# Performance work log

Measured on AMD Instinct MI355X. Metric: run time of the kernel, lower is better.

The kernel has to match this reference:

```python
import jax, jax.numpy as jnp
import numpy as np

D_MODEL = 1024
N_HEADS = 16
D_HEAD = D_MODEL // N_HEADS
L_NS = 64
B = 1
L_S_VAL = 4096


def setup_inputs() -> dict:
    key = jax.random.key(0)
    k0, k1, k2, k3 = jax.random.split(key, 4)
    d = D_MODEL
    x = jax.random.normal(k0, (B, L_S_VAL + L_NS, d), dtype=jnp.float32)
    # xavier-uniform-ish scales
    s_qkv = (2.0 / (d + 3 * d)) ** 0.5
    s_out = (2.0 / (d + d)) ** 0.5
    W_S = jax.random.normal(k1, (d, 3 * d), dtype=jnp.float32) * s_qkv
    W_NS = jax.random.normal(k2, (L_NS, d, 3 * d), dtype=jnp.float32) * s_qkv
    W_out = jax.random.normal(k3, (d, d), dtype=jnp.float32) * s_out
    return {"x": x, "W_S": W_S, "W_NS": W_NS, "W_out": W_out,
            "L_S": L_S_VAL, "query_start": 2048}


def reference(x, W_S, W_NS, W_out, L_S, query_start):
    Bsz, L_total, D = x.shape
    H, Dh = N_HEADS, D_HEAD
    L_q = L_S - query_start

    x_S = x[:, :L_S]                    # (B, L_S, D)
    x_NS = x[:, L_S:L_S + L_NS]         # (B, L_NS, D)

    qkv_S = jnp.einsum('bsd,do->bso', x_S, W_S)        # shared projection
    qkv_NS = jnp.einsum('bnd,ndo->bno', x_NS, W_NS)    # per-NS-token projection

    Q_S, K_S, V_S = jnp.split(qkv_S, 3, axis=-1)
    Q_NS, K_NS, V_NS = jnp.split(qkv_NS, 3, axis=-1)

    Q = jnp.concatenate([Q_S[:, query_start:], Q_NS], axis=1)  # (B, L_q+L_NS, D)
    K = jnp.concatenate([K_S, K_NS], axis=1)                    # (B, L_total, D)
    V = jnp.concatenate([V_S, V_NS], axis=1)

    def to_heads(t):
        return t.reshape(Bsz, t.shape[1], H, Dh).transpose(0, 2, 1, 3)

    Qh, Kh, Vh = to_heads(Q), to_heads(K), to_heads(V)

    q_pos = jnp.arange(query_start, L_S + L_NS)  # (L_q+L_NS,)
    k_pos = jnp.arange(L_total)                  # (L_total,)
    causal_mask = q_pos[:, None] < k_pos[None, :]  # True = masked out

    scale = Dh ** -0.5
    scores = jnp.einsum('bhqd,bhkd->bhqk', Qh, Kh) * scale
    scores = jnp.where(causal_mask[None, None], -jnp.inf, scores)
    attn = jax.nn.softmax(scores, axis=-1)
    attn = jnp.nan_to_num(attn)

    out = jnp.einsum('bhqk,bhkd->bhqd', attn, Vh)
    out = out.transpose(0, 2, 1, 3).reshape(Bsz, L_q + L_NS, D)
    return jnp.einsum('bqd,de->bqe', out, W_out)
```

## Files before the change

kernel.cpp:

```cpp
#include <hip/hip_runtime.h>

typedef __attribute__((ext_vector_type(8))) short bf16x8;
typedef __attribute__((ext_vector_type(4))) float f32x4;

#define MFMA_BF16(a,b,c) __builtin_amdgcn_mfma_f32_16x16x32_bf16(a,b,c,0,0,0)

#define H_ 16
#define DH 64
#define LQ 2112
#define LK 4160
#define QOFF 2048
#define DM 1024
#define NO 3072

__device__ __forceinline__ unsigned short f2bf(float f) {
  union { float f; unsigned u; } v; v.f = f;
  unsigned u = v.u;
  return (unsigned short)((u + 0x7FFFu + ((u >> 16) & 1u)) >> 16);
}

__global__ __launch_bounds__(256) void cvt_x(const float* __restrict__ x,
                                             unsigned short* __restrict__ xb) {
  int i = blockIdx.x * 256 + threadIdx.x;
  float4 f = ((const float4*)x)[i];
  ushort4 o;
  o.x = f2bf(f.x); o.y = f2bf(f.y); o.z = f2bf(f.z); o.w = f2bf(f.w);
  ((ushort4*)xb)[i] = o;
}

__global__ __launch_bounds__(256) void transp_bf(const float* __restrict__ in,
                                                 unsigned short* __restrict__ out,
                                                 int R, int C) {
  __shared__ float t[32][33];
  int c0 = blockIdx.x * 32, r0 = blockIdx.y * 32;
  #pragma unroll
  for (int i = threadIdx.y; i < 32; i += 8)
    t[i][threadIdx.x] = in[(size_t)(r0 + i) * C + c0 + threadIdx.x];
  __syncthreads();
  #pragma unroll
  for (int i = threadIdx.y; i < 32; i += 8)
    out[(size_t)(c0 + i) * R + r0 + threadIdx.x] = f2bf(t[threadIdx.x][i]);
}

__global__ __launch_bounds__(256) void qkv_ns_k(const float* __restrict__ x,
                                                const float* __restrict__ W_NS,
                                                float* __restrict__ qkvNS) {
  int oc = blockIdx.x, dc = blockIdx.y, n = blockIdx.z;
  __shared__ float xs[256];
  xs[threadIdx.x] = x[(size_t)(4096 + n) * DM + dc * 256 + threadIdx.x];
  __syncthreads();
  int o0 = oc * 1024 + threadIdx.x * 4;
  const float* W = W_NS + ((size_t)n * DM + dc * 256) * NO + o0;
  float a0 = 0.f, a1 = 0.f, a2 = 0.f, a3 = 0.f;
  #pragma unroll 4
  for (int d = 0; d < 256; ++d) {
    float xv = xs[d];
    float4 w = *(const float4*)(W + (size_t)d * NO);
    a0 = fmaf(xv, w.x, a0); a1 = fmaf(xv, w.y, a1);
    a2 = fmaf(xv, w.z, a2); a3 = fmaf(xv, w.w, a3);
  }
  float* dst = qkvNS + (size_t)n * NO + o0;
  atomicAdd(dst + 0, a0); atomicAdd(dst + 1, a1);
  atomicAdd(dst + 2, a2); atomicAdd(dst + 3, a3);
}

__global__ __launch_bounds__(256) void scatter_ns(const float* __restrict__ qkvNS,
                                                  unsigned short* __restrict__ Qb,
                                                  unsigned short* __restrict__ Kb,
                                                  unsigned short* __restrict__ Vb) {
  int i = blockIdx.x * 256 + threadIdx.x;
  int n = i / NO, o = i - n * NO;
  float v = qkvNS[i];
  int h = (o & 1023) >> 6, dh = o & 63;
  if (o < 1024)       Qb[((size_t)h * LQ + 2048 + n) * DH + dh] = f2bf(v * 0.125f);
  else if (o < 2048)  Kb[((size_t)h * LK + 4096 + n) * DH + dh] = f2bf(v);
  else                Vb[((size_t)h * LK + 4096 + n) * DH + dh] = f2bf(v);
}

__global__ __launch_bounds__(256) void gemm_qkv(const unsigned short* __restrict__ A,
                                                const unsigned short* __restrict__ BT,
                                                unsigned short* __restrict__ Qb,
                                                unsigned short* __restrict__ Kb,
                                                unsigned short* __restrict__ Vb) {
  __shared__ unsigned short At[128 * 32];
  __shared__ unsigned short Bt[128 * 32];
  int tm = blockIdx.x * 128, tn = blockIdx.y * 128;
  int tid = threadIdx.x, wave = tid >> 6, lane = tid & 63;
  int col = lane & 15, quad = lane >> 4;
  int wr = (wave & 1) * 64, wc = (wave >> 1) * 64;
  int srow = tid >> 2, spart = (tid & 3) * 8;

  f32x4 acc[4][4] = {};

  for (int kb = 0; kb < DM; kb += 32) {
    __syncthreads();
    *(uint4*)&At[srow * 32 + spart]        = *(const uint4*)&A[(size_t)(tm + srow) * DM + kb + spart];
    *(uint4*)&At[(srow + 64) * 32 + spart] = *(const uint4*)&A[(size_t)(tm + srow + 64) * DM + kb + spart];
    *(uint4*)&Bt[srow * 32 + spart]        = *(const uint4*)&BT[(size_t)(tn + srow) * DM + kb + spart];
    *(uint4*)&Bt[(srow + 64) * 32 + spart] = *(const uint4*)&BT[(size_t)(tn + srow + 64) * DM + kb + spart];
    __syncthreads();
    bf16x8 af[4], bfr[4];
    #pragma unroll
    for (int i = 0; i < 4; ++i) {
      af[i]  = *(const bf16x8*)&At[(wr + i * 16 + col) * 32 + quad * 8];
      bfr[i] = *(const bf16x8*)&Bt[(wc + i * 16 + col) * 32 + quad * 8];
    }
    #pragma unroll
    for (int i = 0; i < 4; ++i)
      #pragma unroll
      for (int j = 0; j < 4; ++j)
        acc[i][j] = MFMA_BF16(af[i], bfr[j], acc[i][j]);
  }

  #pragma unroll
  for (int i = 0; i < 4; ++i)
    #pragma unroll
    for (int j = 0; j < 4; ++j)
      #pragma unroll
      for (int r = 0; r < 4; ++r) {
        int m = tm + wr + i * 16 + quad * 4 + r;
        int n = tn + wc + j * 16 + col;
        float v = acc[i][j][r];
        int h = (n & 1023) >> 6, dh = n & 63;
        if (n < 1024) {
          if (m >= QOFF) Qb[((size_t)h * LQ + (m - QOFF)) * DH + dh] = f2bf(v * 0.125f);
        } else if (n < 2048) {
          Kb[((size_t)h * LK + m) * DH + dh] = f2bf(v);
        } else {
          Vb[((size_t)h * LK + m) * DH + dh] = f2bf(v);
        }
      }
}

__global__ __launch_bounds__(256) void attn(const unsigned short* __restrict__ Qb,
                                            const unsigned short* __restrict__ Kb,
                                            const unsigned short* __restrict__ Vb,
                                            unsigned short* __restrict__ Ob) {
  __shared__ unsigned short Kt[32 * 64];
  __shared__ unsigned short Vt[64 * 32];
  __shared__ unsigned short Pt[4][16 * 32];
  int h = blockIdx.y;
  int qb = blockIdx.x * 64;
  int tid = threadIdx.x, wave = tid >> 6, lane = tid & 63;
  int col = lane & 15, quad = lane >> 4;
  const unsigned short* Qh = Qb + (size_t)h * LQ * DH;
  const unsigned short* Kh = Kb + (size_t)h * LK * DH;
  const unsigned short* Vh = Vb + (size_t)h * LK * DH;

  int qrow = qb + wave * 16 + col;
  bf16x8 aq0 = *(const bf16x8*)&Qh[qrow * DH + quad * 8];
  bf16x8 aq1 = *(const bf16x8*)&Qh[qrow * DH + 32 + quad * 8];

  f32x4 oacc[4] = {};
  float m_i[4] = {-3e38f, -3e38f, -3e38f, -3e38f};
  float l_i[4] = {0.f, 0.f, 0.f, 0.f};

  int skl = tid >> 3;
  int sdc = (tid & 7) * 8;

  int nkt = (QOFF + qb + 64) >> 5;
  for (int kt = 0; kt < nkt; ++kt) {
    int kb = kt << 5;
    __syncthreads();
    {
      *(uint4*)&Kt[skl * 64 + sdc] = *(const uint4*)&Kh[(size_t)(kb + skl) * DH + sdc];
      unsigned short tmp[8];
      *(uint4*)tmp = *(const uint4*)&Vh[(size_t)(kb + skl) * DH + sdc];
      #pragma unroll
      for (int j = 0; j < 8; ++j) Vt[(sdc + j) * 32 + skl] = tmp[j];
    }
    __syncthreads();

    f32x4 s0 = {}, s1 = {};
    {
      bf16x8 b00 = *(const bf16x8*)&Kt[col * 64 + quad * 8];
      bf16x8 b01 = *(const bf16x8*)&Kt[col * 64 + 32 + quad * 8];
      bf16x8 b10 = *(const bf16x8*)&Kt[(16 + col) * 64 + quad * 8];
      bf16x8 b11 = *(const bf16x8*)&Kt[(16 + col) * 64 + 32 + quad * 8];
      s0 = MFMA_BF16(aq0, b00, s0); s0 = MFMA_BF16(aq1, b01, s0);
      s1 = MFMA_BF16(aq0, b10, s1); s1 = MFMA_BF16(aq1, b11, s1);
    }

    float alpha[4];
    #pragma unroll
    for (int r = 0; r < 4; ++r) {
      int q = qb + wave * 16 + quad * 4 + r;
      int kmax = QOFF + q;
      float v0 = (kb + col      <= kmax) ? s0[r] : -3e38f;
      float v1 = (kb + 16 + col <= kmax) ? s1[r] : -3e38f;
      float t = fmaxf(v0, v1);
      t = fmaxf(t, __shfl_xor(t, 1));
      t = fmaxf(t, __shfl_xor(t, 2));
      t = fmaxf(t, __shfl_xor(t, 4));
      t = fmaxf(t, __shfl_xor(t, 8));
      float mn = fmaxf(m_i[r], t);
      alpha[r] = __expf(m_i[r] - mn);
      m_i[r] = mn;
      float e0 = __expf(v0 - mn);
      float e1 = __expf(v1 - mn);
      float su = e0 + e1;
      su += __shfl_xor(su, 1);
      su += __shfl_xor(su, 2);
      su += __shfl_xor(su, 4);
      su += __shfl_xor(su, 8);
      l_i[r] = l_i[r] * alpha[r] + su;
      Pt[wave][(quad * 4 + r) * 32 + col]      = f2bf(e0);
      Pt[wave][(quad * 4 + r) * 32 + 16 + col] = f2bf(e1);
    }
    #pragma unroll
    for (int dt = 0; dt < 4; ++dt)
      #pragma unroll
      for (int r = 0; r < 4; ++r) oacc[dt][r] *= alpha[r];

    asm volatile("s_waitcnt lgkmcnt(0)" ::: "memory");
    bf16x8 ap = *(const bf16x8*)&Pt[wave][col * 32 + quad * 8];
    #pragma unroll
    for (int dt = 0; dt < 4; ++dt) {
      bf16x8 bv = *(const bf16x8*)&Vt[(dt * 16 + col) * 32 + quad * 8];
      oacc[dt] = MFMA_BF16(ap, bv, oacc[dt]);
    }
  }

  #pragma unroll
  for (int r = 0; r < 4; ++r) {
    int q = qb + wave * 16 + quad * 4 + r;
    float inv = 1.0f / l_i[r];
    #pragma unroll
    for (int dt = 0; dt < 4; ++dt)
      Ob[(size_t)q * DM + h * DH + dt * 16 + col] = f2bf(oacc[dt][r] * inv);
  }
}

__global__ __launch_bounds__(256) void gemm_out_k(const unsigned short* __restrict__ A,
                                                  const unsigned short* __restrict__ BT,
                                                  float* __restrict__ C) {
  __shared__ unsigned short At[128 * 32];
  __shared__ unsigned short Bt[128 * 32];
  int tm = blockIdx.x * 128, tn = blockIdx.y * 128;
  int tid = threadIdx.x, wave = tid >> 6, lane = tid & 63;
  int col = lane & 15, quad = lane >> 4;
  int wr = (wave & 1) * 64, wc = (wave >> 1) * 64;
  int srow = tid >> 2, spart = (tid & 3) * 8;
  int ar0 = min(tm + srow, LQ - 1);
  int ar1 = min(tm + srow + 64, LQ - 1);

  f32x4 acc[4][4] = {};

  for (int kb = 0; kb < DM; kb += 32) {
    __syncthreads();
    *(uint4*)&At[srow * 32 + spart]        = *(const uint4*)&A[(size_t)ar0 * DM + kb + spart];
    *(uint4*)&At[(srow + 64) * 32 + spart] = *(const uint4*)&A[(size_t)ar1 * DM + kb + spart];
    *(uint4*)&Bt[srow * 32 + spart]        = *(const uint4*)&BT[(size_t)(tn + srow) * DM + kb + spart];
    *(uint4*)&Bt[(srow + 64) * 32 + spart] = *(const uint4*)&BT[(size_t)(tn + srow + 64) * DM + kb + spart];
    __syncthreads();
    bf16x8 af[4], bfr[4];
    #pragma unroll
    for (int i = 0; i < 4; ++i) {
      af[i]  = *(const bf16x8*)&At[(wr + i * 16 + col) * 32 + quad * 8];
      bfr[i] = *(const bf16x8*)&Bt[(wc + i * 16 + col) * 32 + quad * 8];
    }
    #pragma unroll
    for (int i = 0; i < 4; ++i)
      #pragma unroll
      for (int j = 0; j < 4; ++j)
        acc[i][j] = MFMA_BF16(af[i], bfr[j], acc[i][j]);
  }

  #pragma unroll
  for (int i = 0; i < 4; ++i)
    #pragma unroll
    for (int j = 0; j < 4; ++j)
      #pragma unroll
      for (int r = 0; r < 4; ++r) {
        int m = tm + wr + i * 16 + quad * 4 + r;
        int n = tn + wc + j * 16 + col;
        if (m < LQ) C[(size_t)m * DM + n] = acc[i][j][r];
      }
}

extern "C" void kernel_launch(void* const* d_in, const int* in_sizes, int n_in,
                              void* d_out, int out_size, void* d_ws, size_t ws_size,
                              hipStream_t stream) {
  const float* x     = (const float*)d_in[0];
  const float* W_S   = (const float*)d_in[1];
  const float* W_NS  = (const float*)d_in[2];
  const float* W_out = (const float*)d_in[3];
  char* ws = (char*)d_ws;

  unsigned short* xb    = (unsigned short*)(ws + 0);
  unsigned short* WST   = (unsigned short*)(ws + 8519680);
  unsigned short* WOT   = (unsigned short*)(ws + 14811136);
  float*          qkvNS = (float*)(ws + 16908288);
  unsigned short* Qb    = (unsigned short*)(ws + 17694720);
  unsigned short* Kb    = (unsigned short*)(ws + 22020096);
  unsigned short* Vb    = (unsigned short*)(ws + 30539776);
  unsigned short* Ob    = (unsigned short*)(ws + 39059456);
  float* out = (float*)d_out;

  hipMemsetAsync(qkvNS, 0, 64 * NO * sizeof(float), stream);
  cvt_x<<<4160, 256, 0, stream>>>(x, xb);
  transp_bf<<<dim3(96, 32), dim3(32, 8), 0, stream>>>(W_S, WST, 1024, 3072);
  transp_bf<<<dim3(32, 32), dim3(32, 8), 0, stream>>>(W_out, WOT, 1024, 1024);
  qkv_ns_k<<<dim3(3, 4, 64), 256, 0, stream>>>(x, W_NS, qkvNS);
  scatter_ns<<<768, 256, 0, stream>>>(qkvNS, Qb, Kb, Vb);
  gemm_qkv<<<dim3(32, 24), 256, 0, stream>>>(xb, WST, Qb, Kb, Vb);
  attn<<<dim3(33, 16), 256, 0, stream>>>(Qb, Kb, Vb, Ob);
  gemm_out_k<<<dim3(17, 8), 256, 0, stream>>>(Ob, WOT, out);
}
```

Baseline: 1.404 ms.

## Double-buffer attention with direct global-to-LDS loads and pre-transposed V

The attention kernel now uses 64-key tiles, double-buffered in LDS and filled with direct global-to-LDS loads. K and V tiles use XOR-swizzled columns, and the causal mask is applied only on the last tile. The QKV GEMM writes V already transposed per head, so the attention kernel no longer transposes V scalar by scalar in LDS. Both GEMMs switch their tile staging to global_load_lds as well. This is meant to overlap memory with MFMA work and cut LDS staging overhead, at the cost of more LDS use and extra layout complexity.

```diff
diff --git a/kernel.cpp b/kernel.cpp
--- a/kernel.cpp
+++ b/kernel.cpp
@@ -17,6 +17,13 @@
   union { float f; unsigned u; } v; v.f = f;
   unsigned u = v.u;
   return (unsigned short)((u + 0x7FFFu + ((u >> 16) & 1u)) >> 16);
+}
+
+__device__ __forceinline__ void gl_lds16(const unsigned short* g, unsigned short* l) {
+  __builtin_amdgcn_global_load_lds(
+      (const __attribute__((address_space(1))) unsigned int*)g,
+      (__attribute__((address_space(3))) unsigned int*)l,
+      16, 0, 0);
 }
 
 __global__ __launch_bounds__(256) void cvt_x(const float* __restrict__ x,
@@ -67,21 +74,21 @@
 __global__ __launch_bounds__(256) void scatter_ns(const float* __restrict__ qkvNS,
                                                   unsigned short* __restrict__ Qb,
                                                   unsigned short* __restrict__ Kb,
-                                                  unsigned short* __restrict__ Vb) {
+                                                  unsigned short* __restrict__ VbT) {
   int i = blockIdx.x * 256 + threadIdx.x;
   int n = i / NO, o = i - n * NO;
   float v = qkvNS[i];
   int h = (o & 1023) >> 6, dh = o & 63;
   if (o < 1024)       Qb[((size_t)h * LQ + 2048 + n) * DH + dh] = f2bf(v * 0.125f);
   else if (o < 2048)  Kb[((size_t)h * LK + 4096 + n) * DH + dh] = f2bf(v);
-  else                Vb[((size_t)h * LK + 4096 + n) * DH + dh] = f2bf(v);
+  else                VbT[((size_t)(h * 64 + dh)) * LK + 4096 + n] = f2bf(v);
 }
 
 __global__ __launch_bounds__(256) void gemm_qkv(const unsigned short* __restrict__ A,
                                                 const unsigned short* __restrict__ BT,
                                                 unsigned short* __restrict__ Qb,
                                                 unsigned short* __restrict__ Kb,
-                                                unsigned short* __restrict__ Vb) {
+                                                unsigned short* __restrict__ VbT) {
   __shared__ unsigned short At[128 * 32];
   __shared__ unsigned short Bt[128 * 32];
   int tm = blockIdx.x * 128, tn = blockIdx.y * 128;
@@ -94,10 +101,10 @@
 
   for (int kb = 0; kb < DM; kb += 32) {
     __syncthreads();
-    *(uint4*)&At[srow * 32 + spart]        = *(const uint4*)&A[(size_t)(tm + srow) * DM + kb + spart];
-    *(uint4*)&At[(srow + 64) * 32 + spart] = *(const uint4*)&A[(size_t)(tm + srow + 64) * DM + kb + spart];
-    *(uint4*)&Bt[srow * 32 + spart]        = *(const uint4*)&BT[(size_t)(tn + srow) * DM + kb + spart];
-    *(uint4*)&Bt[(srow + 64) * 32 + spart] = *(const uint4*)&BT[(size_t)(tn + srow + 64) * DM + kb + spart];
+    gl_lds16(&A[(size_t)(tm + srow) * DM + kb + spart],       &At[wave * 512]);
+    gl_lds16(&A[(size_t)(tm + srow + 64) * DM + kb + spart],  &At[2048 + wave * 512]);
+    gl_lds16(&BT[(size_t)(tn + srow) * DM + kb + spart],      &Bt[wave * 512]);
+    gl_lds16(&BT[(size_t)(tn + srow + 64) * DM + kb + spart], &Bt[2048 + wave * 512]);
     __syncthreads();
     bf16x8 af[4], bfr[4];
     #pragma unroll
@@ -112,40 +119,60 @@
         acc[i][j] = MFMA_BF16(af[i], bfr[j], acc[i][j]);
   }
 
-  #pragma unroll
-  for (int i = 0; i < 4; ++i)
-    #pragma unroll
-    for (int j = 0; j < 4; ++j)
-      #pragma unroll
-      for (int r = 0; r < 4; ++r) {
-        int m = tm + wr + i * 16 + quad * 4 + r;
+  if (tn >= 2048) {
+    #pragma unroll
+    for (int i = 0; i < 4; ++i)
+      #pragma unroll
+      for (int j = 0; j < 4; ++j) {
         int n = tn + wc + j * 16 + col;
-        float v = acc[i][j][r];
         int h = (n & 1023) >> 6, dh = n & 63;
-        if (n < 1024) {
-          if (m >= QOFF) Qb[((size_t)h * LQ + (m - QOFF)) * DH + dh] = f2bf(v * 0.125f);
-        } else if (n < 2048) {
-          Kb[((size_t)h * LK + m) * DH + dh] = f2bf(v);
-        } else {
-          Vb[((size_t)h * LK + m) * DH + dh] = f2bf(v);
+        int m0 = tm + wr + i * 16 + quad * 4;
+        ushort4 o;
+        o.x = f2bf(acc[i][j][0]); o.y = f2bf(acc[i][j][1]);
+        o.z = f2bf(acc[i][j][2]); o.w = f2bf(acc[i][j][3]);
+        *(ushort4*)&VbT[((size_t)(h * 64 + dh)) * LK + m0] = o;
+      }
+  } else if (tn >= 1024) {
+    #pragma unroll
+    for (int i = 0; i < 4; ++i)
+      #pragma unroll
+      for (int j = 0; j < 4; ++j)
+        #pragma unroll
+        for (int r = 0; r < 4; ++r) {
+          int m = tm + wr + i * 16 + quad * 4 + r;
+          int n = tn + wc + j * 16 + col;
+          int h = (n & 1023) >> 6, dh = n & 63;
+          Kb[((size_t)h * LK + m) * DH + dh] = f2bf(acc[i][j][r]);
         }
-      }
+  } else {
+    #pragma unroll
+    for (int i = 0; i < 4; ++i)
+      #pragma unroll
+      for (int j = 0; j < 4; ++j)
+        #pragma unroll
+        for (int r = 0; r < 4; ++r) {
+          int m = tm + wr + i * 16 + quad * 4 + r;
+          int n = tn + wc + j * 16 + col;
+          int h = (n & 1023) >> 6, dh = n & 63;
+          if (m >= QOFF) Qb[((size_t)h * LQ + (m - QOFF)) * DH + dh] = f2bf(acc[i][j][r] * 0.125f);
+        }
+  }
 }
 
 __global__ __launch_bounds__(256) void attn(const unsigned short* __restrict__ Qb,
                                             const unsigned short* __restrict__ Kb,
-                                            const unsigned short* __restrict__ Vb,
+                                            const unsigned short* __restrict__ VbT,
                                             unsigned short* __restrict__ Ob) {
-  __shared__ unsigned short Kt[32 * 64];
-  __shared__ unsigned short Vt[64 * 32];
-  __shared__ unsigned short Pt[4][16 * 32];
+  __shared__ unsigned short Kt[2][64 * 64];
+  __shared__ unsigned short Vt[2][64 * 64];
+  __shared__ unsigned short Pt[4][16 * 72];
   int h = blockIdx.y;
   int qb = blockIdx.x * 64;
   int tid = threadIdx.x, wave = tid >> 6, lane = tid & 63;
   int col = lane & 15, quad = lane >> 4;
   const unsigned short* Qh = Qb + (size_t)h * LQ * DH;
   const unsigned short* Kh = Kb + (size_t)h * LK * DH;
-  const unsigned short* Vh = Vb + (size_t)h * LK * DH;
+  const unsigned short* Vh = VbT + (size_t)h * 64 * LK;
 
   int qrow = qb + wave * 16 + col;
   bf16x8 aq0 = *(const bf16x8*)&Qh[qrow * DH + quad * 8];
@@ -155,40 +182,51 @@
   float m_i[4] = {-3e38f, -3e38f, -3e38f, -3e38f};
   float l_i[4] = {0.f, 0.f, 0.f, 0.f};
 
-  int skl = tid >> 3;
-  int sdc = (tid & 7) * 8;
-
-  int nkt = (QOFF + qb + 64) >> 5;
+  int row0 = tid >> 3;
+  int sc8  = ((tid & 7) ^ (row0 & 7)) * 8;
+  int xs   = col & 7;
+
+#define STAGE(b, kb_) do { \
+    gl_lds16(&Kh[(size_t)((kb_) + row0) * DH + sc8],        &Kt[b][wave * 512]); \
+    gl_lds16(&Kh[(size_t)((kb_) + row0 + 32) * DH + sc8],   &Kt[b][2048 + wave * 512]); \
+    gl_lds16(&Vh[(size_t)row0 * LK + (kb_) + sc8],          &Vt[b][wave * 512]); \
+    gl_lds16(&Vh[(size_t)(row0 + 32) * LK + (kb_) + sc8],   &Vt[b][2048 + wave * 512]); \
+  } while (0)
+
+  int nkt = 33 + blockIdx.x;
+  STAGE(0, 0);
+  int cur = 0;
   for (int kt = 0; kt < nkt; ++kt) {
-    int kb = kt << 5;
-    __syncthreads();
-    {
-      *(uint4*)&Kt[skl * 64 + sdc] = *(const uint4*)&Kh[(size_t)(kb + skl) * DH + sdc];
-      unsigned short tmp[8];
-      *(uint4*)tmp = *(const uint4*)&Vh[(size_t)(kb + skl) * DH + sdc];
-      #pragma unroll
-      for (int j = 0; j < 8; ++j) Vt[(sdc + j) * 32 + skl] = tmp[j];
-    }
-    __syncthreads();
-
-    f32x4 s0 = {}, s1 = {};
-    {
-      bf16x8 b00 = *(const bf16x8*)&Kt[col * 64 + quad * 8];
-      bf16x8 b01 = *(const bf16x8*)&Kt[col * 64 + 32 + quad * 8];
-      bf16x8 b10 = *(const bf16x8*)&Kt[(16 + col) * 64 + quad * 8];
-      bf16x8 b11 = *(const bf16x8*)&Kt[(16 + col) * 64 + 32 + quad * 8];
-      s0 = MFMA_BF16(aq0, b00, s0); s0 = MFMA_BF16(aq1, b01, s0);
-      s1 = MFMA_BF16(aq0, b10, s1); s1 = MFMA_BF16(aq1, b11, s1);
+    int kb = kt << 6;
+    __syncthreads();
+    if (kt + 1 < nkt) STAGE(cur ^ 1, (kt + 1) << 6);
+
+    const unsigned short* K_ = Kt[cur];
+    const unsigned short* V_ = Vt[cur];
+
+    f32x4 s[4] = {};
+    #pragma unroll
+    for (int f = 0; f < 4; ++f) {
+      int krow = (f * 16 + col) * 64;
+      bf16x8 b0 = *(const bf16x8*)&K_[krow + (quad ^ xs) * 8];
+      bf16x8 b1 = *(const bf16x8*)&K_[krow + (((4 + quad) ^ xs)) * 8];
+      s[f] = MFMA_BF16(aq0, b0, s[f]);
+      s[f] = MFMA_BF16(aq1, b1, s[f]);
     }
 
     float alpha[4];
+    bool lastt = (kt == nkt - 1);
     #pragma unroll
     for (int r = 0; r < 4; ++r) {
-      int q = qb + wave * 16 + quad * 4 + r;
-      int kmax = QOFF + q;
-      float v0 = (kb + col      <= kmax) ? s0[r] : -3e38f;
-      float v1 = (kb + 16 + col <= kmax) ? s1[r] : -3e38f;
-      float t = fmaxf(v0, v1);
+      float v0 = s[0][r], v1 = s[1][r], v2 = s[2][r], v3 = s[3][r];
+      if (lastt) {
+        int kmax = QOFF + qb + wave * 16 + quad * 4 + r;
+        v0 = (kb + col      <= kmax) ? v0 : -3e38f;
+        v1 = (kb + 16 + col <= kmax) ? v1 : -3e38f;
+        v2 = (kb + 32 + col <= kmax) ? v2 : -3e38f;
+        v3 = (kb + 48 + col <= kmax) ? v3 : -3e38f;
+      }
+      float t = fmaxf(fmaxf(v0, v1), fmaxf(v2, v3));
       t = fmaxf(t, __shfl_xor(t, 1));
       t = fmaxf(t, __shfl_xor(t, 2));
       t = fmaxf(t, __shfl_xor(t, 4));
@@ -196,16 +234,19 @@
       float mn = fmaxf(m_i[r], t);
       alpha[r] = __expf(m_i[r] - mn);
       m_i[r] = mn;
-      float e0 = __expf(v0 - mn);
-      float e1 = __expf(v1 - mn);
-      float su = e0 + e1;
+      float e0 = __expf(v0 - mn), e1 = __expf(v1 - mn);
+      float e2 = __expf(v2 - mn), e3 = __expf(v3 - mn);
+      float su = (e0 + e1) + (e2 + e3);
       su += __shfl_xor(su, 1);
       su += __shfl_xor(su, 2);
       su += __shfl_xor(su, 4);
       su += __shfl_xor(su, 8);
       l_i[r] = l_i[r] * alpha[r] + su;
-      Pt[wave][(quad * 4 + r) * 32 + col]      = f2bf(e0);
-      Pt[wave][(quad * 4 + r) * 32 + 16 + col] = f2bf(e1);
+      int pr = (quad * 4 + r) * 72;
+      Pt[wave][pr + col]      = f2bf(e0);
+      Pt[wave][pr + 16 + col] = f2bf(e1);
+      Pt[wave][pr + 32 + col] = f2bf(e2);
+      Pt[wave][pr + 48 + col] = f2bf(e3);
     }
     #pragma unroll
     for (int dt = 0; dt < 4; ++dt)
@@ -213,13 +254,19 @@
       for (int r = 0; r < 4; ++r) oacc[dt][r] *= alpha[r];
 
     asm volatile("s_waitcnt lgkmcnt(0)" ::: "memory");
-    bf16x8 ap = *(const bf16x8*)&Pt[wave][col * 32 + quad * 8];
+    bf16x8 ap0 = *(const bf16x8*)&Pt[wave][col * 72 + quad * 8];
+    bf16x8 ap1 = *(const bf16x8*)&Pt[wave][col * 72 + 32 + quad * 8];
     #pragma unroll
     for (int dt = 0; dt < 4; ++dt) {
-      bf16x8 bv = *(const bf16x8*)&Vt[(dt * 16 + col) * 32 + quad * 8];
-      oacc[dt] = MFMA_BF16(ap, bv, oacc[dt]);
-    }
-  }
+      int dr = (dt * 16 + col) * 64;
+      bf16x8 bv0 = *(const bf16x8*)&V_[dr + (quad ^ xs) * 8];
+      bf16x8 bv1 = *(const bf16x8*)&V_[dr + (((4 + quad) ^ xs)) * 8];
+      oacc[dt] = MFMA_BF16(ap0, bv0, oacc[dt]);
+      oacc[dt] = MFMA_BF16(ap1, bv1, oacc[dt]);
+    }
+    cur ^= 1;
+  }
+#undef STAGE
 
   #pragma unroll
   for (int r = 0; r < 4; ++r) {
@@ -248,10 +295,10 @@
 
   for (int kb = 0; kb < DM; kb += 32) {
     __syncthreads();
-    *(uint4*)&At[srow * 32 + spart]        = *(const uint4*)&A[(size_t)ar0 * DM + kb + spart];
-    *(uint4*)&At[(srow + 64) * 32 + spart] = *(const uint4*)&A[(size_t)ar1 * DM + kb + spart];
-    *(uint4*)&Bt[srow * 32 + spart]        = *(const uint4*)&BT[(size_t)(tn + srow) * DM + kb + spart];
-    *(uint4*)&Bt[(srow + 64) * 32 + spart] = *(const uint4*)&BT[(size_t)(tn + srow + 64) * DM + kb + spart];
+    gl_lds16(&A[(size_t)ar0 * DM + kb + spart],               &At[wave * 512]);
+    gl_lds16(&A[(size_t)ar1 * DM + kb + spart],               &At[2048 + wave * 512]);
+    gl_lds16(&BT[(size_t)(tn + srow) * DM + kb + spart],      &Bt[wave * 512]);
+    gl_lds16(&BT[(size_t)(tn + srow + 64) * DM + kb + spart], &Bt[2048 + wave * 512]);
     __syncthreads();
     bf16x8 af[4], bfr[4];
     #pragma unroll
@@ -293,7 +340,7 @@
   float*          qkvNS = (float*)(ws + 16908288);
   unsigned short* Qb    = (unsigned short*)(ws + 17694720);
   unsigned short* Kb    = (unsigned short*)(ws + 22020096);
-  unsigned short* Vb    = (unsigned short*)(ws + 30539776);
+  unsigned short* VbT   = (unsigned short*)(ws + 30539776);
   unsigned short* Ob    = (unsigned short*)(ws + 39059456);
   float* out = (float*)d_out;
 
@@ -302,8 +349,8 @@
   transp_bf<<<dim3(96, 32), dim3(32, 8), 0, stream>>>(W_S, WST, 1024, 3072);
   transp_bf<<<dim3(32, 32), dim3(32, 8), 0, stream>>>(W_out, WOT, 1024, 1024);
   qkv_ns_k<<<dim3(3, 4, 64), 256, 0, stream>>>(x, W_NS, qkvNS);
-  scatter_ns<<<768, 256, 0, stream>>>(qkvNS, Qb, Kb, Vb);
-  gemm_qkv<<<dim3(32, 24), 256, 0, stream>>>(xb, WST, Qb, Kb, Vb);
-  attn<<<dim3(33, 16), 256, 0, stream>>>(Qb, Kb, Vb, Ob);
+  scatter_ns<<<768, 256, 0, stream>>>(qkvNS, Qb, Kb, VbT);
+  gemm_qkv<<<dim3(32, 24), 256, 0, stream>>>(xb, WST, Qb, Kb, VbT);
+  attn<<<dim3(33, 16), 256, 0, stream>>>(Qb, Kb, VbT, Ob);
   gemm_out_k<<<dim3(17, 8), 256, 0, stream>>>(Ob, WOT, out);
 }
```

Result: faster. 1.274 ms (-9.3%).
